# Performance work log

Measured on AMD Instinct MI355X. Metric: run time of the kernel, lower is better.

The kernel has to match this reference:

```python
import jax, jax.numpy as jnp
import numpy as np

N_NODES = 50000
N_EDGES = 800000
HID = 128
EDGE_DIM = 4
LAYERS = 4
MAX_Z = 100
NUM_GRAPHS = 512


def setup_inputs() -> dict:
    key = jax.random.key(0)
    ks = jax.random.split(key, 16)
    s = lambda k, shape, fan_in: jax.random.normal(k, shape, jnp.float32) / np.sqrt(fan_in)
    inp = {
        "z": jax.random.randint(ks[0], (N_NODES,), 0, MAX_Z + 1),
        "edge_index": jax.random.randint(ks[1], (2, N_EDGES), 0, N_NODES),
        "edge_attr": jax.random.normal(ks[2], (N_EDGES, EDGE_DIM), jnp.float32),
        "batch": jnp.sort(jax.random.randint(ks[3], (N_NODES,), 0, NUM_GRAPHS)),
        "emb": jax.random.normal(ks[4], (MAX_Z + 1, HID), jnp.float32),
        # stacked per-layer params; Linear stored as [in, out]
        "ew1": s(ks[5], (LAYERS, 2 * HID + EDGE_DIM, HID), 2 * HID + EDGE_DIM),
        "eb1": jnp.zeros((LAYERS, HID), jnp.float32),
        "ew2": s(ks[6], (LAYERS, HID, HID), HID),
        "eb2": jnp.zeros((LAYERS, HID), jnp.float32),
        "nw": s(ks[7], (LAYERS, 2 * HID, HID), 2 * HID),
        "nb": jnp.zeros((LAYERS, HID), jnp.float32),
        "rw1": s(ks[8], (HID, HID), HID),
        "rb1": jnp.zeros((HID,), jnp.float32),
        "rw2": s(ks[9], (HID, 1), HID),
        "rb2": jnp.zeros((1,), jnp.float32),
    }
    return inp


def _forward(z, edge_index, edge_attr, batch,
             emb, ew1, eb1, ew2, eb2, nw, nb, rw1, rb1, rw2, rb2):
    silu = jax.nn.silu
    src, dst = edge_index[0], edge_index[1]
    x = emb[z]  # [N, H]
    for l in range(LAYERS):
        m_in = jnp.concatenate([x[src], x[dst], edge_attr], axis=-1)  # [E, 2H+ed]
        h = silu(m_in @ ew1[l] + eb1[l])
        msg = silu(h @ ew2[l] + eb2[l])  # [E, H]
        agg = jax.ops.segment_sum(msg, dst, num_segments=N_NODES)  # scatter-add
        x = silu(jnp.concatenate([x, agg], axis=-1) @ nw[l] + nb[l])
    # segment mean over graphs
    sums = jax.ops.segment_sum(x, batch, num_segments=NUM_GRAPHS)
    counts = jnp.clip(jax.ops.segment_sum(jnp.ones((x.shape[0],), x.dtype), batch,
                                          num_segments=NUM_GRAPHS), 1.0)[:, None]
    g = sums / counts  # [G, H]
    pred = (silu(g @ rw1 + rb1) @ rw2 + rb2)[:, 0]  # [G]
    return pred


def reference(z, edge_index, edge_attr, batch,
              emb, ew1, eb1, ew2, eb2, nw, nb, rw1, rb1, rw2, rb2):
    return _forward(z, edge_index, edge_attr, batch,
                    emb, ew1, eb1, ew2, eb2, nw, nb, rw1, rb1, rw2, rb2)
```

## Files before the change

kernel.cpp:

```cpp
#include <hip/hip_runtime.h>
#include <math.h>

#define HID  128
#define EDIM 4

typedef unsigned short u16;
typedef u16    us8   __attribute__((ext_vector_type(8)));
typedef __bf16 bf16x8 __attribute__((ext_vector_type(8)));
typedef float  f32x4 __attribute__((ext_vector_type(4)));

__device__ __forceinline__ float silu_f(float v) {
    return v * __builtin_amdgcn_rcpf(1.0f + __expf(-v));
}
__device__ __forceinline__ u16 f2bf(float f) {
    unsigned u = __float_as_uint(f);
    unsigned r = u + 0x7fffu + ((u >> 16) & 1u);
    return (u16)(r >> 16);
}
__device__ __forceinline__ u16 f2bf_fast(float f) {
    return (u16)((__float_as_uint(f) + 0x8000u) >> 16);
}
__device__ __forceinline__ unsigned pack_bf2(float a, float b) {
    return ((__float_as_uint(a) + 0x8000u) >> 16) |
           ((__float_as_uint(b) + 0x8000u) & 0xffff0000u);
}
__device__ __forceinline__ float bf2f(u16 s) {
    return __uint_as_float(((unsigned)s) << 16);
}
__device__ __forceinline__ bf16x8 as_bf(us8 v) {
    return __builtin_bit_cast(bf16x8, v);
}

__device__ __forceinline__ void wfrag_gen(const float* __restrict__ w,
        u16* __restrict__ out, int KT, int Kdata, int Kstride,
        int split, int jump, int idx) {
    int lane = idx & 63;
    int f    = (idx >> 6) % (KT * 8);
    int l    = idx / (64 * KT * 8);
    int kt = f >> 3, nt = f & 7;
    int n  = nt * 16 + (lane & 15);
    int k0 = kt * 32 + ((lane >> 4) * 8);
    us8 v;
    #pragma unroll
    for (int j = 0; j < 8; ++j) {
        int k = k0 + j;
        int row = k + (k >= split ? jump : 0);
        v[j] = (row < Kdata) ? f2bf(w[((size_t)l * Kstride + row) * HID + n]) : (u16)0;
    }
    *(us8*)&out[((size_t)(l * KT * 8 + f) * 64 + lane) * 8] = v;
}

#define T1A (4 * 5 * 8 * 64)
#define T1B (4 * 4 * 8 * 64)
#define T2  (4 * 4 * 8 * 64)
#define T3  (4 * 8 * 8 * 64)

__global__ __launch_bounds__(256) void setup_kernel(
        const float* __restrict__ ew1, const float* __restrict__ ew2,
        const float* __restrict__ nw,
        u16* __restrict__ w1af, u16* __restrict__ w1bf,
        u16* __restrict__ w2f, u16* __restrict__ nwf,
        int* __restrict__ cnt, int* __restrict__ cursor,
        float* __restrict__ sums, float* __restrict__ cnts_g, int N, int G) {
    const int BIG = 1 << 30;
    int idx = blockIdx.x * 256 + threadIdx.x;
    if (idx < T1A) { wfrag_gen(ew1, w1af, 5, 260, 260, 128, 128, idx); return; }
    idx -= T1A;
    if (idx < T1B) { wfrag_gen(ew1, w1bf, 4, 260, 260, 0, 128, idx); return; }
    idx -= T1B;
    if (idx < T2) { wfrag_gen(ew2, w2f, 4, 128, 128, BIG, 0, idx); return; }
    idx -= T2;
    if (idx < T3) { wfrag_gen(nw, nwf, 8, 256, 256, BIG, 0, idx); return; }
    idx -= T3;
    if (idx < N) { cnt[idx] = 0; return; }
    idx -= N;
    if (idx < N) { cursor[idx] = 0; return; }
    idx -= N;
    if (idx < G * HID) { sums[idx] = 0.f; return; }
    idx -= G * HID;
    if (idx < G) { cnts_g[idx] = 0.f; return; }
}

__global__ __launch_bounds__(256) void hist_kernel(const int* __restrict__ dst,
        int* __restrict__ cnt, int E) {
    int e = blockIdx.x * 256 + threadIdx.x;
    if (e < E) atomicAdd(&cnt[dst[e]], 1);
}

__global__ __launch_bounds__(1024) void scan_kernel(const int* __restrict__ cnt,
        int* __restrict__ rowptr, int n) {
    __shared__ int s[1024];
    const int t = threadIdx.x;
    const int chunk = (n + 1023) >> 10;
    int lo = t * chunk, hi = lo + chunk;
    if (lo > n) lo = n;
    if (hi > n) hi = n;
    int sum = 0;
    for (int i = lo; i < hi; ++i) sum += cnt[i];
    s[t] = sum;
    __syncthreads();
    for (int off = 1; off < 1024; off <<= 1) {
        int v = (t >= off) ? s[t - off] : 0;
        __syncthreads();
        s[t] += v;
        __syncthreads();
    }
    int run = s[t] - sum;
    for (int i = lo; i < hi; ++i) { rowptr[i] = run; run += cnt[i]; }
    if (t == 1023) rowptr[n] = run;
}

__global__ __launch_bounds__(256) void scatter_kernel(const int* __restrict__ src,
        const int* __restrict__ dst, const float* __restrict__ ea,
        const int* __restrict__ rowptr, int* __restrict__ cursor,
        int* __restrict__ srcS, int* __restrict__ dstS, u16* __restrict__ eaS, int E) {
    int e = blockIdx.x * 256 + threadIdx.x;
    if (e >= E) return;
    int d = dst[e];
    int p = rowptr[d] + atomicAdd(&cursor[d], 1);
    srcS[p] = src[e];
    dstS[p] = d;
    const float* q = &ea[(size_t)e * EDIM];
    ushort4 v;
    v.x = f2bf(q[0]); v.y = f2bf(q[1]); v.z = f2bf(q[2]); v.w = f2bf(q[3]);
    *(ushort4*)&eaS[(size_t)p * 4] = v;
}

__global__ __launch_bounds__(HID) void embed_kernel(const int* __restrict__ z,
        const float* __restrict__ emb, u16* __restrict__ xb,
        float* __restrict__ agg, const int* __restrict__ batch,
        float* __restrict__ counts, int n) {
    int i = blockIdx.x;
    if (i >= n) return;
    int t = threadIdx.x;
    xb[(size_t)i * HID + t] = f2bf(emb[(size_t)z[i] * HID + t]);
    agg[(size_t)i * HID + t] = 0.f;
    if (t == 0) unsafeAtomicAdd(&counts[batch[i]], 1.0f);
}

__global__ __launch_bounds__(256) void y_kernel(
        const u16* __restrict__ xb, const u16* __restrict__ w1bf,
        float* __restrict__ Y, int n) {
    const int t    = threadIdx.x;
    const int i0   = blockIdx.x * 32;
    const int wv   = t >> 6, lane = t & 63;
    const int lrow = lane & 15;
    const int kq   = lane >> 4;
    const int kq8  = kq * 8;

    int iN[2];
    #pragma unroll
    for (int mt = 0; mt < 2; ++mt) {
        int i = i0 + mt * 16 + lrow; if (i >= n) i = n - 1;
        iN[mt] = i;
    }
    f32x4 acc[2][2];
    #pragma unroll
    for (int mt = 0; mt < 2; ++mt)
        #pragma unroll
        for (int nt = 0; nt < 2; ++nt)
            acc[mt][nt] = (f32x4){0.f, 0.f, 0.f, 0.f};

    #pragma unroll
    for (int kt = 0; kt < 4; ++kt) {
        bf16x8 w0 = *(const bf16x8*)&w1bf[((size_t)(kt * 8 + wv * 2 + 0) * 64 + lane) * 8];
        bf16x8 w1 = *(const bf16x8*)&w1bf[((size_t)(kt * 8 + wv * 2 + 1) * 64 + lane) * 8];
        #pragma unroll
        for (int mt = 0; mt < 2; ++mt) {
            bf16x8 a = as_bf(*(const us8*)&xb[(size_t)iN[mt] * HID + kt * 32 + kq8]);
            acc[mt][0] = __builtin_amdgcn_mfma_f32_16x16x32_bf16(w0, a, acc[mt][0], 0, 0, 0);
            acc[mt][1] = __builtin_amdgcn_mfma_f32_16x16x32_bf16(w1, a, acc[mt][1], 0, 0, 0);
        }
    }
    #pragma unroll
    for (int mt = 0; mt < 2; ++mt) {
        int node = i0 + mt * 16 + lrow;
        if (node < n) {
            #pragma unroll
            for (int nt = 0; nt < 2; ++nt)
                *(f32x4*)&Y[(size_t)node * HID + (wv * 2 + nt) * 16 + kq * 4] = acc[mt][nt];
        }
    }
}

__global__ __launch_bounds__(512, 8) void edge_mfma(
        const u16* __restrict__ xin, const int* __restrict__ srcS,
        const int* __restrict__ dstS, const u16* __restrict__ eaS,
        const u16* __restrict__ w1af, const float* __restrict__ b1,
        const u16* __restrict__ w2f, const float* __restrict__ b2,
        const float* __restrict__ Y,
        float* __restrict__ agg, int nE) {
    __shared__ __align__(16) char smem[64 * 132 * 4];
    __shared__ __align__(16) int dsh[64];
    u16*   A = (u16*)smem;
    u16*   H = (u16*)smem;
    float* M = (float*)smem;

    const int t    = threadIdx.x;
    const int e0   = blockIdx.x * 64;
    const int wv   = t >> 6, lane = t & 63;
    const int lrow = lane & 15;
    const int kq   = lane >> 4;
    const int kq8  = kq * 8;
    const int rq   = kq * 4;
    const int h    = wv >> 2;
    const int p    = wv & 3;

    #pragma unroll
    for (int it = 0; it < 2; ++it) {
        int slot = it * 512 + t;
        int row = slot >> 4, ch = slot & 15;
        int e = e0 + row; if (e >= nE) e = nE - 1;
        int node = srcS[e];
        us8 v = *(const us8*)&xin[(size_t)node * HID + ch * 8];
        *(us8*)&A[row * 168 + ch * 8] = v;
    }
    if (t < 64) {
        int e = e0 + t;
        bool valid = e < nE; if (!valid) e = nE - 1;
        dsh[t] = valid ? dstS[e] : -1;
        ushort4 q = *(const ushort4*)&eaS[(size_t)e * 4];
        int base = t * 168 + 128;
        us8 z8 = (us8){0, 0, 0, 0, 0, 0, 0, 0};
        *(us8*)&A[base + 8]  = z8;
        *(us8*)&A[base + 16] = z8;
        *(us8*)&A[base + 24] = z8;
        A[base + 0] = q.x; A[base + 1] = q.y; A[base + 2] = q.z; A[base + 3] = q.w;
        A[base + 4] = 0;   A[base + 5] = 0;   A[base + 6] = 0;   A[base + 7] = 0;
    }
    __syncthreads();

    f32x4 acc[2][2];
    #pragma unroll
    for (int mt = 0; mt < 2; ++mt) {
        int edge = (h * 2 + mt) * 16 + lrow;
        int d = dsh[edge]; if (d < 0) d = 0;
        #pragma unroll
        for (int nt = 0; nt < 2; ++nt) {
            f32x4 bv = *(const f32x4*)&b1[(p * 2 + nt) * 16 + rq];
            f32x4 yv = *(const f32x4*)&Y[(size_t)d * HID + (p * 2 + nt) * 16 + rq];
            acc[mt][nt] = bv + yv;
        }
    }
    #pragma unroll
    for (int kt = 0; kt < 5; ++kt) {
        bf16x8 w0 = *(const bf16x8*)&w1af[((size_t)(kt * 8 + p * 2 + 0) * 64 + lane) * 8];
        bf16x8 w1 = *(const bf16x8*)&w1af[((size_t)(kt * 8 + p * 2 + 1) * 64 + lane) * 8];
        #pragma unroll
        for (int mt = 0; mt < 2; ++mt) {
            bf16x8 a = *(const bf16x8*)&A[((h * 2 + mt) * 16 + lrow) * 168 + kt * 32 + kq8];
            acc[mt][0] = __builtin_amdgcn_mfma_f32_16x16x32_bf16(w0, a, acc[mt][0], 0, 0, 0);
            acc[mt][1] = __builtin_amdgcn_mfma_f32_16x16x32_bf16(w1, a, acc[mt][1], 0, 0, 0);
        }
    }
    __syncthreads();

    #pragma unroll
    for (int mt = 0; mt < 2; ++mt)
        #pragma unroll
        for (int nt = 0; nt < 2; ++nt) {
            uint2 hv;
            hv.x = pack_bf2(silu_f(acc[mt][nt][0]), silu_f(acc[mt][nt][1]));
            hv.y = pack_bf2(silu_f(acc[mt][nt][2]), silu_f(acc[mt][nt][3]));
            int edge = (h * 2 + mt) * 16 + lrow;
            *(uint2*)&H[edge * 136 + (p * 2 + nt) * 16 + rq] = hv;
        }
    __syncthreads();

    f32x4 acc2[2][2];
    #pragma unroll
    for (int nt = 0; nt < 2; ++nt) {
        f32x4 bv = *(const f32x4*)&b2[(p * 2 + nt) * 16 + rq];
        acc2[0][nt] = bv; acc2[1][nt] = bv;
    }
    #pragma unroll
    for (int kt = 0; kt < 4; ++kt) {
        bf16x8 w0 = *(const bf16x8*)&w2f[((size_t)(kt * 8 + p * 2 + 0) * 64 + lane) * 8];
        bf16x8 w1 = *(const bf16x8*)&w2f[((size_t)(kt * 8 + p * 2 + 1) * 64 + lane) * 8];
        #pragma unroll
        for (int mt = 0; mt < 2; ++mt) {
            bf16x8 a = *(const bf16x8*)&H[((h * 2 + mt) * 16 + lrow) * 136 + kt * 32 + kq8];
            acc2[mt][0] = __builtin_amdgcn_mfma_f32_16x16x32_bf16(w0, a, acc2[mt][0], 0, 0, 0);
            acc2[mt][1] = __builtin_amdgcn_mfma_f32_16x16x32_bf16(w1, a, acc2[mt][1], 0, 0, 0);
        }
    }
    __syncthreads();

    #pragma unroll
    for (int mt = 0; mt < 2; ++mt)
        #pragma unroll
        for (int nt = 0; nt < 2; ++nt) {
            f32x4 mv;
            #pragma unroll
            for (int r = 0; r < 4; ++r) mv[r] = silu_f(acc2[mt][nt][r]);
            int edge = (h * 2 + mt) * 16 + lrow;
            *(f32x4*)&M[edge * 132 + (p * 2 + nt) * 16 + rq] = mv;
        }

    {
        int col = p * 32 + (lane & 31);
        int r0  = h * 32 + (lane >> 5) * 16;
        int4 da = *(const int4*)&dsh[r0];
        int4 db = *(const int4*)&dsh[r0 + 4];
        int4 dc = *(const int4*)&dsh[r0 + 8];
        int4 dd = *(const int4*)&dsh[r0 + 12];
        int ds_[16] = {da.x, da.y, da.z, da.w, db.x, db.y, db.z, db.w,
                       dc.x, dc.y, dc.z, dc.w, dd.x, dd.y, dd.z, dd.w};
        float run = 0.f;
        int   cur = ds_[0];
        #pragma unroll
        for (int i = 0; i < 16; ++i) {
            run += M[(r0 + i) * 132 + col];
            int nxt = (i == 15) ? -2 : ds_[i + 1];
            if (cur != nxt) {
                if (cur >= 0)
                    unsafeAtomicAdd(&agg[(size_t)cur * HID + col], run);
                run = 0.f; cur = nxt;
            }
        }
    }
}

__global__ __launch_bounds__(256) void node_mfma(
        u16* __restrict__ xb, float* __restrict__ agg,
        const u16* __restrict__ nwf, const float* __restrict__ nb,
        const int* __restrict__ batch, float* __restrict__ sums,
        int last, int n) {
    const int t    = threadIdx.x;
    const int i0   = blockIdx.x * 32;
    const int wv   = t >> 6, lane = t & 63;
    const int lrow = lane & 15;
    const int kq   = lane >> 4;
    const int kq8  = kq * 8;
    const int rq   = kq * 4;

    int iN[2];
    #pragma unroll
    for (int mt = 0; mt < 2; ++mt) {
        int i = i0 + mt * 16 + lrow; if (i >= n) i = n - 1;
        iN[mt] = i;
    }

    f32x4 acc[2][2];
    {
        float bias0 = nb[wv * 32 + lrow], bias1 = nb[wv * 32 + 16 + lrow];
        #pragma unroll
        for (int mt = 0; mt < 2; ++mt)
            #pragma unroll
            for (int r = 0; r < 4; ++r) {
                acc[mt][0][r] = bias0; acc[mt][1][r] = bias1;
            }
    }
    #pragma unroll
    for (int kt = 0; kt < 4; ++kt) {
        bf16x8 w0 = *(const bf16x8*)&nwf[((size_t)(kt * 8 + wv * 2 + 0) * 64 + lane) * 8];
        bf16x8 w1 = *(const bf16x8*)&nwf[((size_t)(kt * 8 + wv * 2 + 1) * 64 + lane) * 8];
        #pragma unroll
        for (int mt = 0; mt < 2; ++mt) {
            bf16x8 a = as_bf(*(const us8*)&xb[(size_t)iN[mt] * HID + kt * 32 + kq8]);
            acc[mt][0] = __builtin_amdgcn_mfma_f32_16x16x32_bf16(a, w0, acc[mt][0], 0, 0, 0);
            acc[mt][1] = __builtin_amdgcn_mfma_f32_16x16x32_bf16(a, w1, acc[mt][1], 0, 0, 0);
        }
    }
    #pragma unroll
    for (int kt = 4; kt < 8; ++kt) {
        bf16x8 w0 = *(const bf16x8*)&nwf[((size_t)(kt * 8 + wv * 2 + 0) * 64 + lane) * 8];
        bf16x8 w1 = *(const bf16x8*)&nwf[((size_t)(kt * 8 + wv * 2 + 1) * 64 + lane) * 8];
        #pragma unroll
        for (int mt = 0; mt < 2; ++mt) {
            const float* pa = &agg[(size_t)iN[mt] * HID + (kt - 4) * 32 + kq8];
            float4 f0 = *(const float4*)pa;
            float4 f1 = *(const float4*)(pa + 4);
            us8 av;
            av[0] = f2bf_fast(f0.x); av[1] = f2bf_fast(f0.y);
            av[2] = f2bf_fast(f0.z); av[3] = f2bf_fast(f0.w);
            av[4] = f2bf_fast(f1.x); av[5] = f2bf_fast(f1.y);
            av[6] = f2bf_fast(f1.z); av[7] = f2bf_fast(f1.w);
            bf16x8 a = as_bf(av);
            acc[mt][0] = __builtin_amdgcn_mfma_f32_16x16x32_bf16(a, w0, acc[mt][0], 0, 0, 0);
            acc[mt][1] = __builtin_amdgcn_mfma_f32_16x16x32_bf16(a, w1, acc[mt][1], 0, 0, 0);
        }
    }

    if (!last) {
        __syncthreads();
        const float4 z4 = make_float4(0.f, 0.f, 0.f, 0.f);
        #pragma unroll
        for (int kt = 0; kt < 4; ++kt)
            #pragma unroll
            for (int mt = 0; mt < 2; ++mt) {
                float* pa = &agg[(size_t)iN[mt] * HID + kt * 32 + kq8];
                *(float4*)pa = z4; *(float4*)(pa + 4) = z4;
            }
        #pragma unroll
        for (int mt = 0; mt < 2; ++mt)
            #pragma unroll
            for (int nt2 = 0; nt2 < 2; ++nt2)
                #pragma unroll
                for (int r = 0; r < 4; ++r) {
                    int i = i0 + mt * 16 + rq + r;
                    if (i < n)
                        xb[(size_t)i * HID + wv * 32 + nt2 * 16 + lrow] =
                            f2bf_fast(silu_f(acc[mt][nt2][r]));
                }
    } else {
        #pragma unroll
        for (int mt = 0; mt < 2; ++mt)
            #pragma unroll
            for (int nt2 = 0; nt2 < 2; ++nt2)
                #pragma unroll
                for (int r = 0; r < 4; ++r) {
                    int i = i0 + mt * 16 + rq + r;
                    if (i < n) {
                        int b = batch[i];
                        unsafeAtomicAdd(&sums[(size_t)b * HID + wv * 32 + nt2 * 16 + lrow],
                                        silu_f(acc[mt][nt2][r]));
                    }
                }
    }
}

__global__ __launch_bounds__(HID) void readout_kernel(
        const float* __restrict__ sums, const float* __restrict__ counts,
        const float* __restrict__ rw1, const float* __restrict__ rb1,
        const float* __restrict__ rw2, const float* __restrict__ rb2,
        float* __restrict__ pred) {
    __shared__ float gv[HID];
    __shared__ float hv[HID];
    const int g = blockIdx.x;
    const int t = threadIdx.x;
    float c = counts[g];
    if (c < 1.0f) c = 1.0f;
    gv[t] = sums[(size_t)g * HID + t] / c;
    __syncthreads();
    float acc = rb1[t];
    for (int k4 = 0; k4 < 32; ++k4) {
        float4 mv = *(const float4*)&gv[k4 * 4];
        #pragma unroll
        for (int j = 0; j < 4; ++j)
            acc += ((const float*)&mv)[j] * rw1[(size_t)(k4 * 4 + j) * HID + t];
    }
    hv[t] = silu_f(acc) * rw2[t];
    __syncthreads();
    for (int s = HID / 2; s > 0; s >>= 1) {
        if (t < s) hv[t] += hv[t + s];
        __syncthreads();
    }
    if (t == 0) pred[g] = hv[0] + rb2[0];
}

extern "C" void kernel_launch(void* const* d_in, const int* in_sizes, int n_in,
                              void* d_out, int out_size, void* d_ws, size_t ws_size,
                              hipStream_t stream) {
    const int*   z          = (const int*)d_in[0];
    const int*   edge_index = (const int*)d_in[1];
    const float* edge_attr  = (const float*)d_in[2];
    const int*   batch      = (const int*)d_in[3];
    const float* emb        = (const float*)d_in[4];
    const float* ew1        = (const float*)d_in[5];
    const float* eb1        = (const float*)d_in[6];
    const float* ew2        = (const float*)d_in[7];
    const float* eb2        = (const float*)d_in[8];
    const float* nw         = (const float*)d_in[9];
    const float* nb         = (const float*)d_in[10];
    const float* rw1        = (const float*)d_in[11];
    const float* rb1        = (const float*)d_in[12];
    const float* rw2        = (const float*)d_in[13];
    const float* rb2        = (const float*)d_in[14];
    float* pred = (float*)d_out;

    const int N = in_sizes[0];
    const int E = in_sizes[1] / 2;
    const int G = out_size;
    const int* srcI = edge_index;
    const int* dstI = edge_index + E;

    char* base = (char*)d_ws;
    size_t off = 0;
    auto carve = [&](size_t bytes) -> char* {
        char* p = base + off;
        off = (off + bytes + 255) & ~(size_t)255;
        return p;
    };
    float* agg    = (float*)carve((size_t)N * HID * sizeof(float));
    float* sums   = (float*)carve((size_t)G * HID * sizeof(float));
    float* cnts_g = (float*)carve((size_t)G * sizeof(float));
    u16*   xb     = (u16*)carve((size_t)N * HID * sizeof(u16));
    float* Y      = (float*)carve((size_t)N * HID * sizeof(float));
    int*   srcS   = (int*)carve((size_t)(E + 64) * sizeof(int));
    int*   dstS   = (int*)carve((size_t)(E + 64) * sizeof(int));
    u16*   eaS    = (u16*)carve((size_t)(E + 64) * 4 * sizeof(u16));
    int*   rowptr = (int*)carve((size_t)(N + 1) * sizeof(int));
    int*   cursor = (int*)carve((size_t)N * sizeof(int));
    int*   cnt    = (int*)carve((size_t)N * sizeof(int));
    u16*   w1af   = (u16*)carve((size_t)4 * 40 * 512 * sizeof(u16));
    u16*   w1bf   = (u16*)carve((size_t)4 * 32 * 512 * sizeof(u16));
    u16*   w2f    = (u16*)carve((size_t)4 * 32 * 512 * sizeof(u16));
    u16*   nwf    = (u16*)carve((size_t)4 * 64 * 512 * sizeof(u16));

    {
        long long total = (long long)T1A + T1B + T2 + T3 + 2LL * N + (long long)G * HID + G;
        int blocks = (int)((total + 255) / 256);
        setup_kernel<<<blocks, 256, 0, stream>>>(ew1, ew2, nw, w1af, w1bf, w2f, nwf,
                                                 cnt, cursor, sums, cnts_g, N, G);
    }

    hist_kernel<<<(E + 255) / 256, 256, 0, stream>>>(dstI, cnt, E);
    scan_kernel<<<1, 1024, 0, stream>>>(cnt, rowptr, N);
    scatter_kernel<<<(E + 255) / 256, 256, 0, stream>>>(
        srcI, dstI, edge_attr, rowptr, cursor, srcS, dstS, eaS, E);

    embed_kernel<<<N, HID, 0, stream>>>(z, emb, xb, agg, batch, cnts_g, N);

    for (int l = 0; l < 4; ++l) {
        y_kernel<<<(N + 31) / 32, 256, 0, stream>>>(
            xb, w1bf + (size_t)l * 32 * 512, Y, N);
        edge_mfma<<<(E + 63) / 64, 512, 0, stream>>>(
            xb, srcS, dstS, eaS,
            w1af + (size_t)l * 40 * 512, eb1 + (size_t)l * HID,
            w2f + (size_t)l * 32 * 512, eb2 + (size_t)l * HID,
            Y, agg, E);
        node_mfma<<<(N + 31) / 32, 256, 0, stream>>>(
            xb, agg, nwf + (size_t)l * 64 * 512, nb + (size_t)l * HID,
            batch, sums, (l == 3) ? 1 : 0, N);
    }

    readout_kernel<<<G, HID, 0, stream>>>(sums, cnts_g, rw1, rb1, rw2, rb2, pred);
}
```

Before: 1.127 ms.

## Precompute per-node source projection and replace edge first-layer GEMM with gathers

The src-part of the edge first-layer linear is now computed per node (Ys = x @ W_src) in the same kernel as the dst projection. Each edge then gathers fp32 Ys[src] instead of the bf16 x[src] row and runs an MFMA over only the 4-wide edge-attribute block (padded to 32). This cuts edge-level matmul work in the first layer from 5 K-tiles to 1. In exchange, each edge reads a 512-byte fp32 row instead of a 256-byte bf16 row, and an extra N×128 fp32 buffer is written every layer.

```diff
diff --git a/kernel.cpp b/kernel.cpp
--- a/kernel.cpp
+++ b/kernel.cpp
@@ -50,7 +50,8 @@
     *(us8*)&out[((size_t)(l * KT * 8 + f) * 64 + lane) * 8] = v;
 }
 
-#define T1A (4 * 5 * 8 * 64)
+#define T1S (4 * 4 * 8 * 64)
+#define T1T (4 * 1 * 8 * 64)
 #define T1B (4 * 4 * 8 * 64)
 #define T2  (4 * 4 * 8 * 64)
 #define T3  (4 * 8 * 8 * 64)
@@ -58,14 +59,17 @@
 __global__ __launch_bounds__(256) void setup_kernel(
         const float* __restrict__ ew1, const float* __restrict__ ew2,
         const float* __restrict__ nw,
-        u16* __restrict__ w1af, u16* __restrict__ w1bf,
+        u16* __restrict__ w1sf, u16* __restrict__ w1tf,
+        u16* __restrict__ w1bf,
         u16* __restrict__ w2f, u16* __restrict__ nwf,
         int* __restrict__ cnt, int* __restrict__ cursor,
         float* __restrict__ sums, float* __restrict__ cnts_g, int N, int G) {
     const int BIG = 1 << 30;
     int idx = blockIdx.x * 256 + threadIdx.x;
-    if (idx < T1A) { wfrag_gen(ew1, w1af, 5, 260, 260, 128, 128, idx); return; }
-    idx -= T1A;
+    if (idx < T1S) { wfrag_gen(ew1, w1sf, 4, 128, 260, BIG, 0, idx); return; }
+    idx -= T1S;
+    if (idx < T1T) { wfrag_gen(ew1, w1tf, 1, 260, 260, 0, 256, idx); return; }
+    idx -= T1T;
     if (idx < T1B) { wfrag_gen(ew1, w1bf, 4, 260, 260, 0, 128, idx); return; }
     idx -= T1B;
     if (idx < T2) { wfrag_gen(ew2, w2f, 4, 128, 128, BIG, 0, idx); return; }
@@ -138,9 +142,10 @@
     if (t == 0) unsafeAtomicAdd(&counts[batch[i]], 1.0f);
 }
 
-__global__ __launch_bounds__(256) void y_kernel(
-        const u16* __restrict__ xb, const u16* __restrict__ w1bf,
-        float* __restrict__ Y, int n) {
+__global__ __launch_bounds__(256) void ys_kernel(
+        const u16* __restrict__ xb, const u16* __restrict__ w1sf,
+        const u16* __restrict__ w1bf,
+        float* __restrict__ Ys, float* __restrict__ Y, int n) {
     const int t    = threadIdx.x;
     const int i0   = blockIdx.x * 32;
     const int wv   = t >> 6, lane = t & 63;
@@ -154,22 +159,28 @@
         int i = i0 + mt * 16 + lrow; if (i >= n) i = n - 1;
         iN[mt] = i;
     }
-    f32x4 acc[2][2];
+    f32x4 aS[2][2], aB[2][2];
     #pragma unroll
     for (int mt = 0; mt < 2; ++mt)
         #pragma unroll
-        for (int nt = 0; nt < 2; ++nt)
-            acc[mt][nt] = (f32x4){0.f, 0.f, 0.f, 0.f};
+        for (int nt = 0; nt < 2; ++nt) {
+            aS[mt][nt] = (f32x4){0.f, 0.f, 0.f, 0.f};
+            aB[mt][nt] = (f32x4){0.f, 0.f, 0.f, 0.f};
+        }
 
     #pragma unroll
     for (int kt = 0; kt < 4; ++kt) {
-        bf16x8 w0 = *(const bf16x8*)&w1bf[((size_t)(kt * 8 + wv * 2 + 0) * 64 + lane) * 8];
-        bf16x8 w1 = *(const bf16x8*)&w1bf[((size_t)(kt * 8 + wv * 2 + 1) * 64 + lane) * 8];
+        bf16x8 ws0 = *(const bf16x8*)&w1sf[((size_t)(kt * 8 + wv * 2 + 0) * 64 + lane) * 8];
+        bf16x8 ws1 = *(const bf16x8*)&w1sf[((size_t)(kt * 8 + wv * 2 + 1) * 64 + lane) * 8];
+        bf16x8 wb0 = *(const bf16x8*)&w1bf[((size_t)(kt * 8 + wv * 2 + 0) * 64 + lane) * 8];
+        bf16x8 wb1 = *(const bf16x8*)&w1bf[((size_t)(kt * 8 + wv * 2 + 1) * 64 + lane) * 8];
         #pragma unroll
         for (int mt = 0; mt < 2; ++mt) {
             bf16x8 a = as_bf(*(const us8*)&xb[(size_t)iN[mt] * HID + kt * 32 + kq8]);
-            acc[mt][0] = __builtin_amdgcn_mfma_f32_16x16x32_bf16(w0, a, acc[mt][0], 0, 0, 0);
-            acc[mt][1] = __builtin_amdgcn_mfma_f32_16x16x32_bf16(w1, a, acc[mt][1], 0, 0, 0);
+            aS[mt][0] = __builtin_amdgcn_mfma_f32_16x16x32_bf16(ws0, a, aS[mt][0], 0, 0, 0);
+            aS[mt][1] = __builtin_amdgcn_mfma_f32_16x16x32_bf16(ws1, a, aS[mt][1], 0, 0, 0);
+            aB[mt][0] = __builtin_amdgcn_mfma_f32_16x16x32_bf16(wb0, a, aB[mt][0], 0, 0, 0);
+            aB[mt][1] = __builtin_amdgcn_mfma_f32_16x16x32_bf16(wb1, a, aB[mt][1], 0, 0, 0);
         }
     }
     #pragma unroll
@@ -177,21 +188,24 @@
         int node = i0 + mt * 16 + lrow;
         if (node < n) {
             #pragma unroll
-            for (int nt = 0; nt < 2; ++nt)
-                *(f32x4*)&Y[(size_t)node * HID + (wv * 2 + nt) * 16 + kq * 4] = acc[mt][nt];
+            for (int nt = 0; nt < 2; ++nt) {
+                *(f32x4*)&Ys[(size_t)node * HID + (wv * 2 + nt) * 16 + kq * 4] = aS[mt][nt];
+                *(f32x4*)&Y [(size_t)node * HID + (wv * 2 + nt) * 16 + kq * 4] = aB[mt][nt];
+            }
         }
     }
 }
 
 __global__ __launch_bounds__(512, 8) void edge_mfma(
-        const u16* __restrict__ xin, const int* __restrict__ srcS,
-        const int* __restrict__ dstS, const u16* __restrict__ eaS,
-        const u16* __restrict__ w1af, const float* __restrict__ b1,
+        const int* __restrict__ srcS, const int* __restrict__ dstS,
+        const u16* __restrict__ eaS,
+        const u16* __restrict__ w1tf, const float* __restrict__ b1,
         const u16* __restrict__ w2f, const float* __restrict__ b2,
-        const float* __restrict__ Y,
+        const float* __restrict__ Ys, const float* __restrict__ Y,
         float* __restrict__ agg, int nE) {
     __shared__ __align__(16) char smem[64 * 132 * 4];
     __shared__ __align__(16) int dsh[64];
+    __shared__ __align__(16) int ssh[64];
     u16*   A = (u16*)smem;
     u16*   H = (u16*)smem;
     float* M = (float*)smem;
@@ -206,21 +220,13 @@
     const int h    = wv >> 2;
     const int p    = wv & 3;
 
-    #pragma unroll
-    for (int it = 0; it < 2; ++it) {
-        int slot = it * 512 + t;
-        int row = slot >> 4, ch = slot & 15;
-        int e = e0 + row; if (e >= nE) e = nE - 1;
-        int node = srcS[e];
-        us8 v = *(const us8*)&xin[(size_t)node * HID + ch * 8];
-        *(us8*)&A[row * 168 + ch * 8] = v;
-    }
     if (t < 64) {
         int e = e0 + t;
         bool valid = e < nE; if (!valid) e = nE - 1;
         dsh[t] = valid ? dstS[e] : -1;
+        ssh[t] = srcS[e];
         ushort4 q = *(const ushort4*)&eaS[(size_t)e * 4];
-        int base = t * 168 + 128;
+        int base = t * 40;
         us8 z8 = (us8){0, 0, 0, 0, 0, 0, 0, 0};
         *(us8*)&A[base + 8]  = z8;
         *(us8*)&A[base + 16] = z8;
@@ -235,20 +241,21 @@
     for (int mt = 0; mt < 2; ++mt) {
         int edge = (h * 2 + mt) * 16 + lrow;
         int d = dsh[edge]; if (d < 0) d = 0;
+        int s = ssh[edge];
         #pragma unroll
         for (int nt = 0; nt < 2; ++nt) {
             f32x4 bv = *(const f32x4*)&b1[(p * 2 + nt) * 16 + rq];
-            f32x4 yv = *(const f32x4*)&Y[(size_t)d * HID + (p * 2 + nt) * 16 + rq];
-            acc[mt][nt] = bv + yv;
-        }
-    }
-    #pragma unroll
-    for (int kt = 0; kt < 5; ++kt) {
-        bf16x8 w0 = *(const bf16x8*)&w1af[((size_t)(kt * 8 + p * 2 + 0) * 64 + lane) * 8];
-        bf16x8 w1 = *(const bf16x8*)&w1af[((size_t)(kt * 8 + p * 2 + 1) * 64 + lane) * 8];
+            f32x4 yv = *(const f32x4*)&Y [(size_t)d * HID + (p * 2 + nt) * 16 + rq];
+            f32x4 sv = *(const f32x4*)&Ys[(size_t)s * HID + (p * 2 + nt) * 16 + rq];
+            acc[mt][nt] = bv + yv + sv;
+        }
+    }
+    {
+        bf16x8 w0 = *(const bf16x8*)&w1tf[((size_t)(p * 2 + 0) * 64 + lane) * 8];
+        bf16x8 w1 = *(const bf16x8*)&w1tf[((size_t)(p * 2 + 1) * 64 + lane) * 8];
         #pragma unroll
         for (int mt = 0; mt < 2; ++mt) {
-            bf16x8 a = *(const bf16x8*)&A[((h * 2 + mt) * 16 + lrow) * 168 + kt * 32 + kq8];
+            bf16x8 a = *(const bf16x8*)&A[((h * 2 + mt) * 16 + lrow) * 40 + kq8];
             acc[mt][0] = __builtin_amdgcn_mfma_f32_16x16x32_bf16(w0, a, acc[mt][0], 0, 0, 0);
             acc[mt][1] = __builtin_amdgcn_mfma_f32_16x16x32_bf16(w1, a, acc[mt][1], 0, 0, 0);
         }
@@ -487,22 +494,26 @@
     float* cnts_g = (float*)carve((size_t)G * sizeof(float));
     u16*   xb     = (u16*)carve((size_t)N * HID * sizeof(u16));
     float* Y      = (float*)carve((size_t)N * HID * sizeof(float));
+    float* Ys     = (float*)carve((size_t)N * HID * sizeof(float));
     int*   srcS   = (int*)carve((size_t)(E + 64) * sizeof(int));
     int*   dstS   = (int*)carve((size_t)(E + 64) * sizeof(int));
     u16*   eaS    = (u16*)carve((size_t)(E + 64) * 4 * sizeof(u16));
     int*   rowptr = (int*)carve((size_t)(N + 1) * sizeof(int));
     int*   cursor = (int*)carve((size_t)N * sizeof(int));
     int*   cnt    = (int*)carve((size_t)N * sizeof(int));
-    u16*   w1af   = (u16*)carve((size_t)4 * 40 * 512 * sizeof(u16));
+    u16*   w1sf   = (u16*)carve((size_t)4 * 32 * 512 * sizeof(u16));
+    u16*   w1tf   = (u16*)carve((size_t)4 * 8 * 512 * sizeof(u16));
     u16*   w1bf   = (u16*)carve((size_t)4 * 32 * 512 * sizeof(u16));
     u16*   w2f    = (u16*)carve((size_t)4 * 32 * 512 * sizeof(u16));
     u16*   nwf    = (u16*)carve((size_t)4 * 64 * 512 * sizeof(u16));
 
     {
-        long long total = (long long)T1A + T1B + T2 + T3 + 2LL * N + (long long)G * HID + G;
+        long long total = (long long)T1S + T1T + T1B + T2 + T3
+                        + 2LL * N + (long long)G * HID + G;
         int blocks = (int)((total + 255) / 256);
-        setup_kernel<<<blocks, 256, 0, stream>>>(ew1, ew2, nw, w1af, w1bf, w2f, nwf,
-                                                 cnt, cursor, sums, cnts_g, N, G);
+        setup_kernel<<<blocks, 256, 0, stream>>>(ew1, ew2, nw, w1sf, w1tf, w1bf,
+                                                 w2f, nwf, cnt, cursor,
+                                                 sums, cnts_g, N, G);
     }
 
     hist_kernel<<<(E + 255) / 256, 256, 0, stream>>>(dstI, cnt, E);
@@ -513,13 +524,14 @@
     embed_kernel<<<N, HID, 0, stream>>>(z, emb, xb, agg, batch, cnts_g, N);
 
     for (int l = 0; l < 4; ++l) {
-        y_kernel<<<(N + 31) / 32, 256, 0, stream>>>(
-            xb, w1bf + (size_t)l * 32 * 512, Y, N);
+        ys_kernel<<<(N + 31) / 32, 256, 0, stream>>>(
+            xb, w1sf + (size_t)l * 32 * 512, w1bf + (size_t)l * 32 * 512,
+            Ys, Y, N);
         edge_mfma<<<(E + 63) / 64, 512, 0, stream>>>(
-            xb, srcS, dstS, eaS,
-            w1af + (size_t)l * 40 * 512, eb1 + (size_t)l * HID,
+            srcS, dstS, eaS,
+            w1tf + (size_t)l * 8 * 512, eb1 + (size_t)l * HID,
             w2f + (size_t)l * 32 * 512, eb2 + (size_t)l * HID,
-            Y, agg, E);
+            Ys, Y, agg, E);
         node_mfma<<<(N + 31) / 32, 256, 0, stream>>>(
             xb, agg, nwf + (size_t)l * 64 * 512, nb + (size_t)l * HID,
             batch, sums, (l == 3) ? 1 : 0, N);
```

New measurement: 1.124 ms. Within noise of the previous version (-0.3%).
